# Kernel optimization log

Hardware: AMD Instinct MI355X
Metric: run time of the kernel (lower is better)

The kernel has to match this reference:

```python
import jax, jax.numpy as jnp
import numpy as np
from jax import lax

T, B, I, H = 512, 256, 128, 256

def setup_inputs() -> dict:
    key = jax.random.key(0)
    k1, k2, k3, k4 = jax.random.split(key, 4)
    x = jax.random.normal(k1, (T, B, I), dtype=jnp.float32)
    h0 = jnp.zeros((B, H), dtype=jnp.float32)
    Wi = jax.random.normal(k2, (H, I), dtype=jnp.float32) * (1.0 / np.sqrt(I))
    Wh = jax.random.normal(k3, (H, H), dtype=jnp.float32) * (1.0 / np.sqrt(H))
    bh = jax.random.normal(k4, (H,), dtype=jnp.float32) * 0.01
    return {"x": x, "h0": h0, "Wi": Wi, "Wh": Wh, "bh": bh}

def reference(x, h0, Wi, Wh, bh):
    # Precompute input projection for all timesteps: [T, B, H]
    xi = jnp.einsum("tbi,hi->tbh", x, Wi) + bh
    def step(h, xi_t):
        h_new = jnp.tanh(xi_t + h @ Wh.T)
        return h_new, h_new
    _, hs = lax.scan(step, h0, xi)
    return hs  # [T, B, H] hidden states, matching torch stack(out[1:])
```

## Files before the change

kernel.cpp:

```cpp
#include <hip/hip_runtime.h>
#include <hip/hip_bf16.h>
#include <math.h>

#define TT 512
#define BB 256
#define II 128
#define HH 256

__global__ __launch_bounds__(256) void proj_kernel(
    const float* __restrict__ x, const float* __restrict__ Wi,
    const float* __restrict__ bh, float* __restrict__ out)
{
    __shared__ float xt[128][68];
    __shared__ float wt[128][64];

    const int tid = threadIdx.x;
    const int m0 = blockIdx.x * 64;
    const int j0 = blockIdx.y * 64;

    {
        const int r  = tid & 63;
        const int kc = tid >> 6;
        const float* xsrc = x  + (size_t)(m0 + r) * II + kc * 32;
        const float* wsrc = Wi + (size_t)(j0 + r) * II + kc * 32;
#pragma unroll
        for (int u = 0; u < 8; ++u) {
            float4 v = *(const float4*)(xsrc + u * 4);
            int k = kc * 32 + u * 4;
            xt[k + 0][r] = v.x; xt[k + 1][r] = v.y;
            xt[k + 2][r] = v.z; xt[k + 3][r] = v.w;
        }
#pragma unroll
        for (int u = 0; u < 8; ++u) {
            float4 v = *(const float4*)(wsrc + u * 4);
            int k = kc * 32 + u * 4;
            wt[k + 0][r] = v.x; wt[k + 1][r] = v.y;
            wt[k + 2][r] = v.z; wt[k + 3][r] = v.w;
        }
    }
    __syncthreads();

    const int ty = tid >> 4, tx = tid & 15;
    const int r0 = ty * 4, c0 = tx * 4;
    float acc[4][4] = {};
#pragma unroll 4
    for (int k = 0; k < 128; ++k) {
        float4 a = *(const float4*)&xt[k][r0];
        float4 b = *(const float4*)&wt[k][c0];
        float av[4] = {a.x, a.y, a.z, a.w};
        float bv[4] = {b.x, b.y, b.z, b.w};
#pragma unroll
        for (int i = 0; i < 4; ++i)
#pragma unroll
            for (int j = 0; j < 4; ++j)
                acc[i][j] += av[i] * bv[j];
    }

    float4 bias = *(const float4*)(bh + j0 + c0);
    float bvv[4] = {bias.x, bias.y, bias.z, bias.w};
#pragma unroll
    for (int i = 0; i < 4; ++i) {
        float4 o;
        o.x = acc[i][0] + bvv[0];
        o.y = acc[i][1] + bvv[1];
        o.z = acc[i][2] + bvv[2];
        o.w = acc[i][3] + bvv[3];
        *(float4*)(out + (size_t)(m0 + r0 + i) * HH + j0 + c0) = o;
    }
}


#define RNN_CHUNK(CNT, A0,A1,B0,B1,C0,C1,D0,D1, H0,H1) \
        "s_waitcnt lgkmcnt(" CNT ")\n" \
        "v_pk_fma_f32 v[32:33], v[" A0 "], v[" H0 "], v[32:33]\n" \
        "v_pk_fma_f32 v[34:35], v[" B0 "], v[" H0 "], v[34:35]\n" \
        "v_pk_fma_f32 v[36:37], v[" C0 "], v[" H0 "], v[36:37]\n" \
        "v_pk_fma_f32 v[38:39], v[" D0 "], v[" H0 "], v[38:39]\n" \
        "v_pk_fma_f32 v[32:33], v[" A1 "], v[" H1 "], v[32:33]\n" \
        "v_pk_fma_f32 v[34:35], v[" B1 "], v[" H1 "], v[34:35]\n" \
        "v_pk_fma_f32 v[36:37], v[" C1 "], v[" H1 "], v[36:37]\n" \
        "v_pk_fma_f32 v[38:39], v[" D1 "], v[" H1 "], v[38:39]\n"

#define RNN_BODY(XN, XC) \
         \
        "ds_read_b128 v[40:43], v16\n" \
        "ds_read_b128 v[44:47], v16 offset:16\n" \
        "ds_read_b128 v[48:51], v16 offset:32\n" \
        "ds_read_b128 v[52:55], v16 offset:48\n" \
        "ds_read_b128 v[56:59], v16 offset:64\n" \
        "ds_read_b128 v[60:63], v16 offset:80\n" \
        "ds_read_b128 v[64:67], v16 offset:96\n" \
        "ds_read_b128 v[68:71], v16 offset:112\n" \
         \
        "global_load_dword " XN ", v18, %[iob]\n" \
        "v_add_u32 v18, 0x40000, v18\n" \
        "v_min_u32 v18, %[viomax], v18\n" \
         \
        "s_waitcnt lgkmcnt(7)\n" \
        "v_pk_mul_f32 v[32:33], v[72:73],   v[40:41]\n" \
        "v_pk_mul_f32 v[34:35], v[104:105], v[40:41]\n" \
        "v_pk_mul_f32 v[36:37], v[136:137], v[40:41]\n" \
        "v_pk_mul_f32 v[38:39], v[168:169], v[40:41]\n" \
        "v_pk_fma_f32 v[32:33], v[74:75],   v[42:43], v[32:33]\n" \
        "v_pk_fma_f32 v[34:35], v[106:107], v[42:43], v[34:35]\n" \
        "v_pk_fma_f32 v[36:37], v[138:139], v[42:43], v[36:37]\n" \
        "v_pk_fma_f32 v[38:39], v[170:171], v[42:43], v[38:39]\n" \
        RNN_CHUNK("6","76:77","78:79","108:109","110:111","140:141","142:143","172:173","174:175","44:45","46:47") \
        RNN_CHUNK("5","80:81","82:83","112:113","114:115","144:145","146:147","176:177","178:179","48:49","50:51") \
        RNN_CHUNK("4","84:85","86:87","116:117","118:119","148:149","150:151","180:181","182:183","52:53","54:55") \
        RNN_CHUNK("3","88:89","90:91","120:121","122:123","152:153","154:155","184:185","186:187","56:57","58:59") \
        RNN_CHUNK("2","92:93","94:95","124:125","126:127","156:157","158:159","188:189","190:191","60:61","62:63") \
        RNN_CHUNK("1","96:97","98:99","128:129","130:131","160:161","162:163","192:193","194:195","64:65","66:67") \
        RNN_CHUNK("0","100:101","102:103","132:133","134:135","164:165","166:167","196:197","198:199","68:69","70:71") \
         \
        "v_add_f32 v26, v32, v33\n" \
        "v_add_f32 v27, v34, v35\n" \
        "v_add_f32 v28, v36, v37\n" \
        "v_add_f32 v29, v38, v39\n" \
         \
        "v_add_f32 v26, v26, v26 quad_perm:[1,0,3,2] row_mask:0xf bank_mask:0xf\n" \
        "v_add_f32 v27, v27, v27 quad_perm:[1,0,3,2] row_mask:0xf bank_mask:0xf\n" \
        "v_add_f32 v28, v28, v28 quad_perm:[1,0,3,2] row_mask:0xf bank_mask:0xf\n" \
        "v_add_f32 v29, v29, v29 quad_perm:[1,0,3,2] row_mask:0xf bank_mask:0xf\n" \
        "v_add_f32 v26, v26, v26 quad_perm:[2,3,0,1] row_mask:0xf bank_mask:0xf\n" \
        "v_add_f32 v27, v27, v27 quad_perm:[2,3,0,1] row_mask:0xf bank_mask:0xf\n" \
        "v_add_f32 v28, v28, v28 quad_perm:[2,3,0,1] row_mask:0xf bank_mask:0xf\n" \
        "v_add_f32 v29, v29, v29 quad_perm:[2,3,0,1] row_mask:0xf bank_mask:0xf\n" \
        "v_add_f32 v26, v26, v26 row_ror:8 row_mask:0xf bank_mask:0xf\n" \
        "v_add_f32 v27, v27, v27 row_ror:8 row_mask:0xf bank_mask:0xf\n" \
        "v_add_f32 v28, v28, v28 row_ror:8 row_mask:0xf bank_mask:0xf\n" \
        "v_add_f32 v29, v29, v29 row_ror:8 row_mask:0xf bank_mask:0xf\n" \
         \
        "v_cndmask_b32 v30, v26, v27, %[m0]\n" \
        "v_cndmask_b32 v31, v28, v29, %[m0]\n" \
        "v_cndmask_b32 v30, v30, v31, %[m1]\n" \
         \
        "s_waitcnt vmcnt(2)\n" \
        "v_add_f32 v30, v30, " XC "\n" \
         \
        "v_mul_f32 v19, 0x4038aa3b, v30\n" \
        "v_exp_f32 v19, v19\n" \
        "s_nop 1\n" \
        "v_add_f32 v19, 1.0, v19\n" \
        "v_rcp_f32 v19, v19\n" \
        "s_nop 1\n" \
        "v_fma_f32 v30, -2.0, v19, 1.0\n" \
         \
        "ds_write_b32 v17, v30\n" \
        "global_store_dword v23, v30, %[iob]\n" \
        "v_add_u32 v23, 0x40000, v23\n" \
        "s_waitcnt lgkmcnt(0)\n" \
        "s_barrier\n" \
        "v_xor_b32 v16, 0x800, v16\n" \
        "v_xor_b32 v17, 0x800, v17\n"

__global__ __launch_bounds__(512, 2) void rec_kernel(
    const float* __restrict__ Wh, const float* __restrict__ h0,
    float* __restrict__ io)
{
    __shared__ float hbuf[864];

    const int tid  = threadIdx.x;
    const int b    = blockIdx.x;
    const int lane = tid & 63;
    const int q    = tid >> 6;
    const int kg   = (lane & 3) | ((lane >> 1) & 4);
    const int cg   = ((lane >> 2) & 1) | ((lane >> 3) & 6);
    const int col0 = 32 * q + 4 * cg;
    const int col  = col0 + (kg & 3);

    const float* wp  = Wh + (size_t)col0 * HH + kg * 32;
    const float* iob = io + (size_t)b * HH;
    unsigned hbase = (unsigned)(size_t)&hbuf[0];
    unsigned hvr = hbase + kg * 144;
    unsigned hvw = (kg < 4)
        ? hbase + 0x800 + q * 144 + (4 * cg + kg) * 4
        : hbase + 0xD00 + cg * 16 + (kg & 3) * 4;
    unsigned vio = (unsigned)(col * 4);
    unsigned viomax = vio + 511u * 0x40000u;
    unsigned long long m0 = __ballot((lane & 1) != 0);
    unsigned long long m1 = __ballot((lane & 2) != 0);

    if (tid < HH) hbuf[(tid >> 5) * 36 + (tid & 31)] = h0[(size_t)b * HH + tid];
    __syncthreads();

    asm volatile(
        "global_load_dwordx4 v[72:75],   %[wp], off\n"
        "global_load_dwordx4 v[76:79],   %[wp], off offset:16\n"
        "global_load_dwordx4 v[80:83],   %[wp], off offset:32\n"
        "global_load_dwordx4 v[84:87],   %[wp], off offset:48\n"
        "global_load_dwordx4 v[88:91],   %[wp], off offset:64\n"
        "global_load_dwordx4 v[92:95],   %[wp], off offset:80\n"
        "global_load_dwordx4 v[96:99],   %[wp], off offset:96\n"
        "global_load_dwordx4 v[100:103], %[wp], off offset:112\n"
        "global_load_dwordx4 v[104:107], %[wp], off offset:1024\n"
        "global_load_dwordx4 v[108:111], %[wp], off offset:1040\n"
        "global_load_dwordx4 v[112:115], %[wp], off offset:1056\n"
        "global_load_dwordx4 v[116:119], %[wp], off offset:1072\n"
        "global_load_dwordx4 v[120:123], %[wp], off offset:1088\n"
        "global_load_dwordx4 v[124:127], %[wp], off offset:1104\n"
        "global_load_dwordx4 v[128:131], %[wp], off offset:1120\n"
        "global_load_dwordx4 v[132:135], %[wp], off offset:1136\n"
        "global_load_dwordx4 v[136:139], %[wp], off offset:2048\n"
        "global_load_dwordx4 v[140:143], %[wp], off offset:2064\n"
        "global_load_dwordx4 v[144:147], %[wp], off offset:2080\n"
        "global_load_dwordx4 v[148:151], %[wp], off offset:2096\n"
        "global_load_dwordx4 v[152:155], %[wp], off offset:2112\n"
        "global_load_dwordx4 v[156:159], %[wp], off offset:2128\n"
        "global_load_dwordx4 v[160:163], %[wp], off offset:2144\n"
        "global_load_dwordx4 v[164:167], %[wp], off offset:2160\n"
        "global_load_dwordx4 v[168:171], %[wp], off offset:3072\n"
        "global_load_dwordx4 v[172:175], %[wp], off offset:3088\n"
        "global_load_dwordx4 v[176:179], %[wp], off offset:3104\n"
        "global_load_dwordx4 v[180:183], %[wp], off offset:3120\n"
        "global_load_dwordx4 v[184:187], %[wp], off offset:3136\n"
        "global_load_dwordx4 v[188:191], %[wp], off offset:3152\n"
        "global_load_dwordx4 v[192:195], %[wp], off offset:3168\n"
        "global_load_dwordx4 v[196:199], %[wp], off offset:3184\n"
        "v_mov_b32 v16, %[hvr]\n"
        "v_mov_b32 v17, %[hvw]\n"
        "v_mov_b32 v18, %[vio]\n"
        "v_mov_b32 v23, %[vio]\n"
        "global_load_dword v21, v18, %[iob]\n"
        "v_add_u32 v18, 0x40000, v18\n"
        "s_movk_i32 s82, 0x100\n"
        "s_waitcnt vmcnt(0)\n"
        "LTOP_%=:\n"
        RNN_BODY("v20", "v21")
        RNN_BODY("v21", "v20")
        "s_sub_u32 s82, s82, 1\n"
        "s_cmp_lg_u32 s82, 0\n"
        "s_cbranch_scc1 LTOP_%=\n"
        :
        : [wp] "v"(wp), [iob] "s"(iob),
          [hvr] "v"(hvr), [hvw] "v"(hvw), [vio] "v"(vio),
          [viomax] "v"(viomax), [m0] "s"(m0), [m1] "s"(m1)
        : "memory", "scc", "s82",
          "v16","v17","v18","v19","v20","v21","v22","v23",
          "v24","v25","v26","v27","v28","v29","v30","v31",
          "v32","v33","v34","v35","v36","v37","v38","v39",
          "v40","v41","v42","v43","v44","v45","v46","v47",
          "v48","v49","v50","v51","v52","v53","v54","v55",
          "v56","v57","v58","v59","v60","v61","v62","v63",
          "v64","v65","v66","v67","v68","v69","v70","v71",
          "v72","v73","v74","v75","v76","v77","v78","v79",
          "v80","v81","v82","v83","v84","v85","v86","v87",
          "v88","v89","v90","v91","v92","v93","v94","v95",
          "v96","v97","v98","v99","v100","v101","v102","v103",
          "v104","v105","v106","v107","v108","v109","v110","v111",
          "v112","v113","v114","v115","v116","v117","v118","v119",
          "v120","v121","v122","v123","v124","v125","v126","v127",
          "v128","v129","v130","v131","v132","v133","v134","v135",
          "v136","v137","v138","v139","v140","v141","v142","v143",
          "v144","v145","v146","v147","v148","v149","v150","v151",
          "v152","v153","v154","v155","v156","v157","v158","v159",
          "v160","v161","v162","v163","v164","v165","v166","v167",
          "v168","v169","v170","v171","v172","v173","v174","v175",
          "v176","v177","v178","v179","v180","v181","v182","v183",
          "v184","v185","v186","v187","v188","v189","v190","v191",
          "v192","v193","v194","v195","v196","v197","v198","v199");
}

extern "C" void kernel_launch(void* const* d_in, const int* in_sizes, int n_in,
                              void* d_out, int out_size, void* d_ws, size_t ws_size,
                              hipStream_t stream) {
    const float* x  = (const float*)d_in[0];
    const float* h0 = (const float*)d_in[1];
    const float* Wi = (const float*)d_in[2];
    const float* Wh = (const float*)d_in[3];
    const float* bh = (const float*)d_in[4];
    float* out = (float*)d_out;

    dim3 pgrid(TT * BB / 64, HH / 64);
    proj_kernel<<<pgrid, 256, 0, stream>>>(x, Wi, bh, out);
    rec_kernel<<<BB, 512, 0, stream>>>(Wh, h0, out);
}
```

Baseline: 400.6 us.

## Fold tanh exponent scale into weights and input projection, trim recurrence step

Multiplies the input projection output and the register-resident recurrent weights by 2*log2(e) ahead of time, so each step skips the scaling multiply before v_exp and can use shorter nops. The ds_write of the new hidden state is masked to half the lanes, which removes the separate scratch write area, and the read-pointer toggle moves earlier to shorten the step tail. The projection GEMM loop is also restructured to batch eight LDS loads before the FMAs. The intermediate buffer now holds scaled values, which slightly changes rounding.

```diff
diff --git a/kernel.cpp b/kernel.cpp
--- a/kernel.cpp
+++ b/kernel.cpp
@@ -6,6 +6,8 @@
 #define BB 256
 #define II 128
 #define HH 256
+
+#define TANH_S 2.885390043258667f
 
 __global__ __launch_bounds__(256) void proj_kernel(
     const float* __restrict__ x, const float* __restrict__ Wi,
@@ -41,31 +43,40 @@
     __syncthreads();
 
     const int ty = tid >> 4, tx = tid & 15;
-    const int r0 = ty * 4, c0 = tx * 4;
+    const float* xp = &xt[0][ty * 4];
+    const float* wp = &wt[0][tx * 4];
     float acc[4][4] = {};
-#pragma unroll 4
-    for (int k = 0; k < 128; ++k) {
-        float4 a = *(const float4*)&xt[k][r0];
-        float4 b = *(const float4*)&wt[k][c0];
-        float av[4] = {a.x, a.y, a.z, a.w};
-        float bv[4] = {b.x, b.y, b.z, b.w};
-#pragma unroll
-        for (int i = 0; i < 4; ++i)
-#pragma unroll
-            for (int j = 0; j < 4; ++j)
-                acc[i][j] += av[i] * bv[j];
+
+#pragma unroll
+    for (int kk = 0; kk < 128; kk += 8) {
+        float4 av[8], bv[8];
+#pragma unroll
+        for (int u = 0; u < 8; ++u) {
+            av[u] = *(const float4*)(xp + (size_t)(kk + u) * 68);
+            bv[u] = *(const float4*)(wp + (size_t)(kk + u) * 64);
+        }
+#pragma unroll
+        for (int u = 0; u < 8; ++u) {
+            float a4[4] = {av[u].x, av[u].y, av[u].z, av[u].w};
+            float b4[4] = {bv[u].x, bv[u].y, bv[u].z, bv[u].w};
+#pragma unroll
+            for (int i = 0; i < 4; ++i)
+#pragma unroll
+                for (int j = 0; j < 4; ++j)
+                    acc[i][j] += a4[i] * b4[j];
+        }
     }
 
-    float4 bias = *(const float4*)(bh + j0 + c0);
+    float4 bias = *(const float4*)(bh + j0 + tx * 4);
     float bvv[4] = {bias.x, bias.y, bias.z, bias.w};
 #pragma unroll
     for (int i = 0; i < 4; ++i) {
         float4 o;
-        o.x = acc[i][0] + bvv[0];
-        o.y = acc[i][1] + bvv[1];
-        o.z = acc[i][2] + bvv[2];
-        o.w = acc[i][3] + bvv[3];
-        *(float4*)(out + (size_t)(m0 + r0 + i) * HH + j0 + c0) = o;
+        o.x = (acc[i][0] + bvv[0]) * TANH_S;
+        o.y = (acc[i][1] + bvv[1]) * TANH_S;
+        o.z = (acc[i][2] + bvv[2]) * TANH_S;
+        o.w = (acc[i][3] + bvv[3]) * TANH_S;
+        *(float4*)(out + (size_t)(m0 + ty * 4 + i) * HH + j0 + tx * 4) = o;
     }
 }
 
@@ -92,6 +103,7 @@
         "ds_read_b128 v[64:67], v16 offset:96\n" \
         "ds_read_b128 v[68:71], v16 offset:112\n" \
          \
+        "v_xor_b32 v16, 0x800, v16\n" \
         "global_load_dword " XN ", v18, %[iob]\n" \
         "v_add_u32 v18, 0x40000, v18\n" \
         "v_min_u32 v18, %[viomax], v18\n" \
@@ -138,21 +150,24 @@
         "s_waitcnt vmcnt(2)\n" \
         "v_add_f32 v30, v30, " XC "\n" \
          \
-        "v_mul_f32 v19, 0x4038aa3b, v30\n" \
-        "v_exp_f32 v19, v19\n" \
-        "s_nop 1\n" \
+        "v_exp_f32 v19, v30\n" \
+        "s_nop 0\n" \
         "v_add_f32 v19, 1.0, v19\n" \
         "v_rcp_f32 v19, v19\n" \
-        "s_nop 1\n" \
+        "s_nop 0\n" \
         "v_fma_f32 v30, -2.0, v19, 1.0\n" \
          \
+        "s_and_saveexec_b64 s[84:85], %[msk]\n" \
         "ds_write_b32 v17, v30\n" \
+        "s_mov_b64 exec, s[84:85]\n" \
+        "v_xor_b32 v17, 0x800, v17\n" \
+         \
         "global_store_dword v23, v30, %[iob]\n" \
         "v_add_u32 v23, 0x40000, v23\n" \
         "s_waitcnt lgkmcnt(0)\n" \
-        "s_barrier\n" \
-        "v_xor_b32 v16, 0x800, v16\n" \
-        "v_xor_b32 v17, 0x800, v17\n"
+        "s_barrier\n"
+
+#define SCALE_PAIR(P) "v_pk_mul_f32 v[" P "], v[" P "], v[26:27]\n"
 
 __global__ __launch_bounds__(512, 2) void rec_kernel(
     const float* __restrict__ Wh, const float* __restrict__ h0,
@@ -173,13 +188,12 @@
     const float* iob = io + (size_t)b * HH;
     unsigned hbase = (unsigned)(size_t)&hbuf[0];
     unsigned hvr = hbase + kg * 144;
-    unsigned hvw = (kg < 4)
-        ? hbase + 0x800 + q * 144 + (4 * cg + kg) * 4
-        : hbase + 0xD00 + cg * 16 + (kg & 3) * 4;
+    unsigned hvw = hbase + 0x800 + q * 144 + (4 * cg + (kg & 3)) * 4;
     unsigned vio = (unsigned)(col * 4);
     unsigned viomax = vio + 511u * 0x40000u;
     unsigned long long m0 = __ballot((lane & 1) != 0);
     unsigned long long m1 = __ballot((lane & 2) != 0);
+    unsigned long long msk = __ballot(kg < 4);
 
     if (tid < HH) hbuf[(tid >> 5) * 36 + (tid & 31)] = h0[(size_t)b * HH + tid];
     __syncthreads();
@@ -225,6 +239,24 @@
         "v_add_u32 v18, 0x40000, v18\n"
         "s_movk_i32 s82, 0x100\n"
         "s_waitcnt vmcnt(0)\n"
+        "v_mov_b32 v26, 0x4038aa3b\n"
+        "v_mov_b32 v27, 0x4038aa3b\n"
+        SCALE_PAIR("72:73")   SCALE_PAIR("74:75")   SCALE_PAIR("76:77")   SCALE_PAIR("78:79")
+        SCALE_PAIR("80:81")   SCALE_PAIR("82:83")   SCALE_PAIR("84:85")   SCALE_PAIR("86:87")
+        SCALE_PAIR("88:89")   SCALE_PAIR("90:91")   SCALE_PAIR("92:93")   SCALE_PAIR("94:95")
+        SCALE_PAIR("96:97")   SCALE_PAIR("98:99")   SCALE_PAIR("100:101") SCALE_PAIR("102:103")
+        SCALE_PAIR("104:105") SCALE_PAIR("106:107") SCALE_PAIR("108:109") SCALE_PAIR("110:111")
+        SCALE_PAIR("112:113") SCALE_PAIR("114:115") SCALE_PAIR("116:117") SCALE_PAIR("118:119")
+        SCALE_PAIR("120:121") SCALE_PAIR("122:123") SCALE_PAIR("124:125") SCALE_PAIR("126:127")
+        SCALE_PAIR("128:129") SCALE_PAIR("130:131") SCALE_PAIR("132:133") SCALE_PAIR("134:135")
+        SCALE_PAIR("136:137") SCALE_PAIR("138:139") SCALE_PAIR("140:141") SCALE_PAIR("142:143")
+        SCALE_PAIR("144:145") SCALE_PAIR("146:147") SCALE_PAIR("148:149") SCALE_PAIR("150:151")
+        SCALE_PAIR("152:153") SCALE_PAIR("154:155") SCALE_PAIR("156:157") SCALE_PAIR("158:159")
+        SCALE_PAIR("160:161") SCALE_PAIR("162:163") SCALE_PAIR("164:165") SCALE_PAIR("166:167")
+        SCALE_PAIR("168:169") SCALE_PAIR("170:171") SCALE_PAIR("172:173") SCALE_PAIR("174:175")
+        SCALE_PAIR("176:177") SCALE_PAIR("178:179") SCALE_PAIR("180:181") SCALE_PAIR("182:183")
+        SCALE_PAIR("184:185") SCALE_PAIR("186:187") SCALE_PAIR("188:189") SCALE_PAIR("190:191")
+        SCALE_PAIR("192:193") SCALE_PAIR("194:195") SCALE_PAIR("196:197") SCALE_PAIR("198:199")
         "LTOP_%=:\n"
         RNN_BODY("v20", "v21")
         RNN_BODY("v21", "v20")
@@ -234,8 +266,8 @@
         :
         : [wp] "v"(wp), [iob] "s"(iob),
           [hvr] "v"(hvr), [hvw] "v"(hvw), [vio] "v"(vio),
-          [viomax] "v"(viomax), [m0] "s"(m0), [m1] "s"(m1)
-        : "memory", "scc", "s82",
+          [viomax] "v"(viomax), [m0] "s"(m0), [m1] "s"(m1), [msk] "s"(msk)
+        : "memory", "scc", "s82", "s84", "s85",
           "v16","v17","v18","v19","v20","v21","v22","v23",
           "v24","v25","v26","v27","v28","v29","v30","v31",
           "v32","v33","v34","v35","v36","v37","v38","v39",
```

Measured after the change: 397.4 us. About the same (-0.8%).
